# Optimization experiments

Hardware: AMD Instinct MI355X
Metric: run time of the kernel (lower is better)

The kernel has to match this reference:

```python
import jax, jax.numpy as jnp
import numpy as np

INPUT_DIM, HIDDEN_DIM, OUTPUT_DIM = 13, 256, 80


def setup_inputs() -> dict:
    key = jax.random.key(0)
    ks = jax.random.split(key, 5)
    x = jax.random.normal(ks[0], (64, 2048, INPUT_DIM), dtype=jnp.float32)
    # Xavier-uniform init like init_weights(); biases zero.
    def xavier(k, fan_in, fan_out):
        lim = np.sqrt(6.0 / (fan_in + fan_out)).astype(np.float32)
        return jax.random.uniform(k, (fan_in, fan_out), jnp.float32, -lim, lim)
    W1 = xavier(ks[1], INPUT_DIM, HIDDEN_DIM)
    W2 = xavier(ks[2], HIDDEN_DIM, HIDDEN_DIM)
    W3 = xavier(ks[3], HIDDEN_DIM, HIDDEN_DIM)
    W4 = xavier(ks[4], HIDDEN_DIM, OUTPUT_DIM)
    b1 = jnp.zeros((HIDDEN_DIM,), jnp.float32)
    b2 = jnp.zeros((HIDDEN_DIM,), jnp.float32)
    b3 = jnp.zeros((HIDDEN_DIM,), jnp.float32)
    b4 = jnp.zeros((OUTPUT_DIM,), jnp.float32)
    return {"x": x, "W1": W1, "b1": b1, "W2": W2, "b2": b2,
            "W3": W3, "b3": b3, "W4": W4, "b4": b4}


def reference(x, W1, b1, W2, b2, W3, b3, W4, b4):
    # Original loops over timesteps, but each timestep is an identical
    # Linear+ReLU stack -> collapse batch*seq into one batched matmul chain.
    h = jax.nn.relu(jnp.einsum('bsi,ih->bsh', x, W1) + b1)   # encoder L1
    h = jax.nn.relu(jnp.einsum('bsh,hk->bsk', h, W2) + b2)   # encoder L2
    h = jax.nn.relu(jnp.einsum('bsh,hk->bsk', h, W3) + b3)   # decoder L1
    out = jnp.einsum('bsh,ho->bso', h, W4) + b4              # decoder L2 (no ReLU)
    return out
```

## Files before the change

kernel.cpp:

```cpp
#include <hip/hip_runtime.h>


typedef _Float16 half_t;
typedef _Float16 half8 __attribute__((ext_vector_type(8)));
typedef float f32x16 __attribute__((ext_vector_type(16)));
typedef unsigned int uint4v __attribute__((ext_vector_type(4)));
typedef int int2v __attribute__((ext_vector_type(2)));

#define M_TOTAL (64*2048)

__global__ void prep_w(const float* __restrict__ W1, const float* __restrict__ W2,
                       const float* __restrict__ W3, const float* __restrict__ W4,
                       half_t* __restrict__ wp) {
    int tid = blockIdx.x * 256 + threadIdx.x;
    if (tid >= 312 * 512) return;
    int blk = tid >> 9, r = tid & 511;
    int lane = r >> 3, j = r & 7;
    const float* W; int K, N, nt, ks;
    if (blk < 8)        { W = W1; K = 13;  N = 256; nt = blk;              ks = 0; }
    else if (blk < 136) { W = W2; K = 256; N = 256; nt = (blk-8) >> 4;     ks = (blk-8) & 15; }
    else if (blk < 264) { W = W3; K = 256; N = 256; nt = (blk-136) >> 4;   ks = (blk-136) & 15; }
    else                { W = W4; K = 256; N = 80;  nt = (blk-264) >> 4;   ks = (blk-264) & 15; }
    int k = ks * 16 + (lane >> 5) * 8 + j;
    int n = nt * 32 + (lane & 31);
    float v = (k < K && n < N) ? W[k * N + n] : 0.f;
    wp[tid] = (half_t)v;
}


__device__ __forceinline__ unsigned int pkrtz(float a, float b) {
    auto p = __builtin_amdgcn_cvt_pkrtz(a, b);
    return __builtin_bit_cast(unsigned int, p);
}

typedef const __attribute__((address_space(1))) unsigned int guint_t;
typedef __attribute__((address_space(3))) unsigned int luint_t;

__device__ __forceinline__ void stage_strip(const half_t* __restrict__ g,
                                            half_t* l, int bytes, int tid) {
    const char* gc = (const char*)g;
    char* lc = (char*)l;
    const int go = tid * 16;
    const int lo = (tid >> 6) << 10;
#pragma unroll
    for (int r = 0; r < bytes; r += 4096) {
        __builtin_amdgcn_global_load_lds((guint_t*)(gc + r + go),
                                         (luint_t*)(lc + r + lo), 16, 0, 0);
    }
}

__device__ __forceinline__ int strip_off(int s) {
    if (s == 0)  return 0;
    if (s <= 4)  return (8   + (s - 1) * 32) * 512;
    if (s <= 8)  return (136 + (s - 5) * 32) * 512;
    if (s == 9)  return 264 * 512;
    return 296 * 512;
}

template <bool RELU>
__device__ __forceinline__ void repack_s(const f32x16& acc, int s,
                                         const float* biasnt, bool hi,
                                         unsigned int* Bw)
{
    float v[8];
#pragma unroll
    for (int q = 0; q < 8; ++q) {
        int f = (q & 3) + 8 * (q >> 2) + (hi ? 4 : 0);
        float t = acc[8 * s + q] + biasnt[16 * s + f];
        v[q] = RELU ? fmaxf(t, 0.f) : t;
    }
    unsigned int P0 = pkrtz(v[0], v[1]);
    unsigned int P1 = pkrtz(v[2], v[3]);
    unsigned int P2 = pkrtz(v[4], v[5]);
    unsigned int P3 = pkrtz(v[6], v[7]);
    int2v r02 = __builtin_amdgcn_permlane32_swap((int)P0, (int)P2, false, false);
    int2v r13 = __builtin_amdgcn_permlane32_swap((int)P1, (int)P3, false, false);
    Bw[0] = (unsigned int)r02.x;
    Bw[1] = (unsigned int)r13.x;
    Bw[2] = (unsigned int)r02.y;
    Bw[3] = (unsigned int)r13.y;
}

#define MFMA16(a, b, c) __builtin_amdgcn_mfma_f32_32x32x16_f16((a), (b), (c), 0, 0, 0)

__device__ __forceinline__ half8 bw_cast(const unsigned int* w) {
    uint4v t = { w[0], w[1], w[2], w[3] };
    return __builtin_bit_cast(half8, t);
}

template <bool RELU>
__device__ __forceinline__ void dense_phase(const half_t* sb,
                                            const unsigned int (&Bin)[2][16][4],
                                            unsigned int (&Bout)[2][16][4],
                                            int ntbase, const float* biasL,
                                            int lane, bool hi)
{
    f32x16 acc00 = {}, acc01 = {}, acc10 = {}, acc11 = {};
    __builtin_amdgcn_s_setprio(1);
#pragma unroll
    for (int ks = 0; ks < 16; ++ks) {
        half8 a0 = *(const half8*)(sb + ((ks * 64 + lane) << 3));
        half8 a1 = *(const half8*)(sb + 16 * 512 + ((ks * 64 + lane) << 3));
        half8 b0 = bw_cast(Bin[0][ks]);
        half8 b1 = bw_cast(Bin[1][ks]);
        acc00 = MFMA16(a0, b0, acc00);
        acc01 = MFMA16(a0, b1, acc01);
        acc10 = MFMA16(a1, b0, acc10);
        acc11 = MFMA16(a1, b1, acc11);
    }
    __builtin_amdgcn_s_setprio(0);
#pragma unroll
    for (int s = 0; s < 2; ++s) {
        repack_s<RELU>(acc00, s, biasL + ntbase * 32, hi, Bout[0][2 * ntbase + s]);
        repack_s<RELU>(acc01, s, biasL + ntbase * 32, hi, Bout[1][2 * ntbase + s]);
        repack_s<RELU>(acc10, s, biasL + (ntbase + 1) * 32, hi, Bout[0][2 * (ntbase + 1) + s]);
        repack_s<RELU>(acc11, s, biasL + (ntbase + 1) * 32, hi, Bout[1][2 * (ntbase + 1) + s]);
    }
}

__device__ __forceinline__ void out_phase2(const half_t* sb,
                                           const unsigned int (&Bin)[2][16][4],
                                           const float* bias4, float* __restrict__ out,
                                           int mb, int lane, bool hi)
{
    f32x16 acc00 = {}, acc01 = {}, acc10 = {}, acc11 = {};
    __builtin_amdgcn_s_setprio(1);
#pragma unroll
    for (int ks = 0; ks < 16; ++ks) {
        half8 a0 = *(const half8*)(sb + ((ks * 64 + lane) << 3));
        half8 a1 = *(const half8*)(sb + 16 * 512 + ((ks * 64 + lane) << 3));
        half8 b0 = bw_cast(Bin[0][ks]);
        half8 b1 = bw_cast(Bin[1][ks]);
        acc00 = MFMA16(a0, b0, acc00);
        acc01 = MFMA16(a0, b1, acc01);
        acc10 = MFMA16(a1, b0, acc10);
        acc11 = MFMA16(a1, b1, acc11);
    }
    __builtin_amdgcn_s_setprio(0);
#pragma unroll
    for (int ntL = 0; ntL < 2; ++ntL) {
#pragma unroll
        for (int g = 0; g < 2; ++g) {
            const f32x16& acc = ntL == 0 ? (g == 0 ? acc00 : acc01)
                                         : (g == 0 ? acc10 : acc11);
            float* orow = out + (long)(mb + g * 32 + (lane & 31)) * 80 + ntL * 32;
#pragma unroll
            for (int reg = 0; reg < 16; ++reg) {
                int rr = (reg & 3) + 8 * (reg >> 2) + (hi ? 4 : 0);
                orow[rr] = acc[reg] + bias4[ntL * 32 + rr];
            }
        }
    }
}

__device__ __forceinline__ void out_phase1(const half_t* sb,
                                           const unsigned int (&Bin)[2][16][4],
                                           const float* bias42, float* __restrict__ out,
                                           int mb, int lane, bool hi)
{
    f32x16 acc0 = {}, acc1 = {};
    __builtin_amdgcn_s_setprio(1);
#pragma unroll
    for (int ks = 0; ks < 16; ++ks) {
        half8 a = *(const half8*)(sb + ((ks * 64 + lane) << 3));
        acc0 = MFMA16(a, bw_cast(Bin[0][ks]), acc0);
        acc1 = MFMA16(a, bw_cast(Bin[1][ks]), acc1);
    }
    __builtin_amdgcn_s_setprio(0);
#pragma unroll
    for (int g = 0; g < 2; ++g) {
        const f32x16& acc = g == 0 ? acc0 : acc1;
        float* orow = out + (long)(mb + g * 32 + (lane & 31)) * 80 + 64;
#pragma unroll
        for (int reg = 0; reg < 8; ++reg) {
            int rr = (reg & 3) + 8 * (reg >> 2) + (hi ? 4 : 0);
            orow[rr] = acc[reg] + bias42[rr];
        }
    }
}

__global__ __attribute__((amdgpu_flat_work_group_size(256, 256), amdgpu_waves_per_eu(1)))
void mlp_mfma(
    const float* __restrict__ x, const half_t* __restrict__ wp,
    const float* __restrict__ b1, const float* __restrict__ b2,
    const float* __restrict__ b3, const float* __restrict__ b4,
    float* __restrict__ out)
{
    __shared__ half_t wbuf[2][16384];
    __shared__ float  bias_lds[864];

    const int tid  = threadIdx.x;
    const int lane = tid & 63;
    const int wave = tid >> 6;
    const bool hi  = lane >= 32;

    stage_strip(wp + strip_off(0), wbuf[0], 8192, tid);

    bias_lds[tid] = b1[tid];
    bias_lds[256 + tid] = b2[tid];
    bias_lds[512 + tid] = b3[tid];
    if (tid < 96) bias_lds[768 + tid] = (tid < 80) ? b4[tid] : 0.f;

    __syncthreads();

#pragma unroll
    for (int h = 0; h < 2; ++h) {
        const int mb = blockIdx.x * 512 + h * 256 + wave * 64;

        unsigned int Bx[2][4];
#pragma unroll
        for (int g = 0; g < 2; ++g) {
            const float* xp = x + (long)(mb + g * 32 + (lane & 31)) * 13;
            float xv[8];
            if (!hi) {
#pragma unroll
                for (int j = 0; j < 8; ++j) xv[j] = xp[j];
            } else {
#pragma unroll
                for (int j = 0; j < 5; ++j) xv[j] = xp[8 + j];
                xv[5] = xv[6] = xv[7] = 0.f;
            }
            Bx[g][0] = pkrtz(xv[0], xv[1]);
            Bx[g][1] = pkrtz(xv[2], xv[3]);
            Bx[g][2] = pkrtz(xv[4], xv[5]);
            Bx[g][3] = pkrtz(xv[6], xv[7]);
        }

        unsigned int BA[2][16][4], BB[2][16][4];

        {
            const int p = h * 11;
            stage_strip(wp + strip_off(1), wbuf[(p + 1) & 1], 32768, tid);
            __builtin_amdgcn_sched_barrier(0);
            const half_t* sb = &wbuf[p & 1][0];
            half8 bx0 = bw_cast(Bx[0]);
            half8 bx1 = bw_cast(Bx[1]);
#pragma unroll
            for (int nt = 0; nt < 8; ++nt) {
                half8 a = *(const half8*)(sb + nt * 512 + (lane << 3));
                f32x16 acc0 = {}, acc1 = {};
                acc0 = MFMA16(a, bx0, acc0);
                acc1 = MFMA16(a, bx1, acc1);
#pragma unroll
                for (int s = 0; s < 2; ++s) {
                    repack_s<true>(acc0, s, bias_lds + nt * 32, hi, BB[0][2 * nt + s]);
                    repack_s<true>(acc1, s, bias_lds + nt * 32, hi, BB[1][2 * nt + s]);
                }
            }
            __syncthreads();
        }

#pragma unroll
        for (int i = 0; i < 4; ++i) {
            const int p = h * 11 + 1 + i;
            stage_strip(wp + strip_off(2 + i), wbuf[(p + 1) & 1], 32768, tid);
            __builtin_amdgcn_sched_barrier(0);
            dense_phase<true>(&wbuf[p & 1][0], BB, BA, 2 * i, bias_lds + 256, lane, hi);
            __syncthreads();
        }

#pragma unroll
        for (int i = 0; i < 4; ++i) {
            const int p = h * 11 + 5 + i;
            stage_strip(wp + strip_off(6 + i), wbuf[(p + 1) & 1],
                        (6 + i == 9) ? 32768 : 32768, tid);
            __builtin_amdgcn_sched_barrier(0);
            dense_phase<true>(&wbuf[p & 1][0], BA, BB, 2 * i, bias_lds + 512, lane, hi);
            __syncthreads();
        }

        {
            const int p = h * 11 + 9;
            stage_strip(wp + strip_off(10), wbuf[(p + 1) & 1], 16384, tid);
            __builtin_amdgcn_sched_barrier(0);
            out_phase2(&wbuf[p & 1][0], BB, bias_lds + 768, out, mb, lane, hi);
            __syncthreads();
        }

        {
            const int p = h * 11 + 10;
            if (h == 0) {
                stage_strip(wp + strip_off(0), wbuf[(p + 1) & 1], 8192, tid);
                __builtin_amdgcn_sched_barrier(0);
            }
            out_phase1(&wbuf[p & 1][0], BB, bias_lds + 768 + 64, out, mb, lane, hi);
            __syncthreads();
        }
    }
}


extern "C" void kernel_launch(void* const* d_in, const int* in_sizes, int n_in,
                              void* d_out, int out_size, void* d_ws, size_t ws_size,
                              hipStream_t stream) {
    const float* x  = (const float*)d_in[0];
    const float* W1 = (const float*)d_in[1];
    const float* b1 = (const float*)d_in[2];
    const float* W2 = (const float*)d_in[3];
    const float* b2 = (const float*)d_in[4];
    const float* W3 = (const float*)d_in[5];
    const float* b3 = (const float*)d_in[6];
    const float* W4 = (const float*)d_in[7];
    const float* b4 = (const float*)d_in[8];
    float* out = (float*)d_out;

    half_t* wp = (half_t*)d_ws;

    hipLaunchKernelGGL(prep_w, dim3(624), dim3(256), 0, stream, W1, W2, W3, W4, wp);
    hipLaunchKernelGGL(mlp_mfma, dim3(M_TOTAL / 512), dim3(256), 0, stream,
                       x, wp, b1, b2, b3, b4, out);
}
```

Baseline: 60.58 us.

## Halve rows per block and allow two waves per EU for occupancy

Removes the two-half loop so each block handles 256 rows instead of 512. The grid doubles and the waves-per-EU hint rises from 1 to 2, so two blocks can share a CU and hide weight-staging and barrier latency. In exchange, each block stages the full weight strips from global memory, doubling L2 weight traffic. The register budget per wave is also halved, which risks spilling the large ping-pong activation arrays held in registers.

```diff
diff --git a/kernel.cpp b/kernel.cpp
--- a/kernel.cpp
+++ b/kernel.cpp
@@ -179,7 +179,7 @@
     }
 }
 
-__global__ __attribute__((amdgpu_flat_work_group_size(256, 256), amdgpu_waves_per_eu(1)))
+__global__ __attribute__((amdgpu_flat_work_group_size(256, 256), amdgpu_waves_per_eu(2)))
 void mlp_mfma(
     const float* __restrict__ x, const half_t* __restrict__ wp,
     const float* __restrict__ b1, const float* __restrict__ b2,
@@ -193,6 +193,7 @@
     const int lane = tid & 63;
     const int wave = tid >> 6;
     const bool hi  = lane >= 32;
+    const int mb   = blockIdx.x * 256 + wave * 64;
 
     stage_strip(wp + strip_off(0), wbuf[0], 8192, tid);
 
@@ -201,92 +202,77 @@
     bias_lds[512 + tid] = b3[tid];
     if (tid < 96) bias_lds[768 + tid] = (tid < 80) ? b4[tid] : 0.f;
 
+    unsigned int Bx[2][4];
+#pragma unroll
+    for (int g = 0; g < 2; ++g) {
+        const float* xp = x + (long)(mb + g * 32 + (lane & 31)) * 13;
+        float xv[8];
+        if (!hi) {
+#pragma unroll
+            for (int j = 0; j < 8; ++j) xv[j] = xp[j];
+        } else {
+#pragma unroll
+            for (int j = 0; j < 5; ++j) xv[j] = xp[8 + j];
+            xv[5] = xv[6] = xv[7] = 0.f;
+        }
+        Bx[g][0] = pkrtz(xv[0], xv[1]);
+        Bx[g][1] = pkrtz(xv[2], xv[3]);
+        Bx[g][2] = pkrtz(xv[4], xv[5]);
+        Bx[g][3] = pkrtz(xv[6], xv[7]);
+    }
+
     __syncthreads();
 
-#pragma unroll
-    for (int h = 0; h < 2; ++h) {
-        const int mb = blockIdx.x * 512 + h * 256 + wave * 64;
-
-        unsigned int Bx[2][4];
-#pragma unroll
-        for (int g = 0; g < 2; ++g) {
-            const float* xp = x + (long)(mb + g * 32 + (lane & 31)) * 13;
-            float xv[8];
-            if (!hi) {
-#pragma unroll
-                for (int j = 0; j < 8; ++j) xv[j] = xp[j];
-            } else {
-#pragma unroll
-                for (int j = 0; j < 5; ++j) xv[j] = xp[8 + j];
-                xv[5] = xv[6] = xv[7] = 0.f;
+    unsigned int BA[2][16][4], BB[2][16][4];
+
+    {
+        stage_strip(wp + strip_off(1), wbuf[1], 32768, tid);
+        __builtin_amdgcn_sched_barrier(0);
+        const half_t* sb = &wbuf[0][0];
+        half8 bx0 = bw_cast(Bx[0]);
+        half8 bx1 = bw_cast(Bx[1]);
+#pragma unroll
+        for (int nt = 0; nt < 8; ++nt) {
+            half8 a = *(const half8*)(sb + nt * 512 + (lane << 3));
+            f32x16 acc0 = {}, acc1 = {};
+            acc0 = MFMA16(a, bx0, acc0);
+            acc1 = MFMA16(a, bx1, acc1);
+#pragma unroll
+            for (int s = 0; s < 2; ++s) {
+                repack_s<true>(acc0, s, bias_lds + nt * 32, hi, BB[0][2 * nt + s]);
+                repack_s<true>(acc1, s, bias_lds + nt * 32, hi, BB[1][2 * nt + s]);
             }
-            Bx[g][0] = pkrtz(xv[0], xv[1]);
-            Bx[g][1] = pkrtz(xv[2], xv[3]);
-            Bx[g][2] = pkrtz(xv[4], xv[5]);
-            Bx[g][3] = pkrtz(xv[6], xv[7]);
-        }
-
-        unsigned int BA[2][16][4], BB[2][16][4];
-
-        {
-            const int p = h * 11;
-            stage_strip(wp + strip_off(1), wbuf[(p + 1) & 1], 32768, tid);
-            __builtin_amdgcn_sched_barrier(0);
-            const half_t* sb = &wbuf[p & 1][0];
-            half8 bx0 = bw_cast(Bx[0]);
-            half8 bx1 = bw_cast(Bx[1]);
-#pragma unroll
-            for (int nt = 0; nt < 8; ++nt) {
-                half8 a = *(const half8*)(sb + nt * 512 + (lane << 3));
-                f32x16 acc0 = {}, acc1 = {};
-                acc0 = MFMA16(a, bx0, acc0);
-                acc1 = MFMA16(a, bx1, acc1);
-#pragma unroll
-                for (int s = 0; s < 2; ++s) {
-                    repack_s<true>(acc0, s, bias_lds + nt * 32, hi, BB[0][2 * nt + s]);
-                    repack_s<true>(acc1, s, bias_lds + nt * 32, hi, BB[1][2 * nt + s]);
-                }
-            }
-            __syncthreads();
-        }
-
-#pragma unroll
-        for (int i = 0; i < 4; ++i) {
-            const int p = h * 11 + 1 + i;
-            stage_strip(wp + strip_off(2 + i), wbuf[(p + 1) & 1], 32768, tid);
-            __builtin_amdgcn_sched_barrier(0);
-            dense_phase<true>(&wbuf[p & 1][0], BB, BA, 2 * i, bias_lds + 256, lane, hi);
-            __syncthreads();
-        }
-
-#pragma unroll
-        for (int i = 0; i < 4; ++i) {
-            const int p = h * 11 + 5 + i;
-            stage_strip(wp + strip_off(6 + i), wbuf[(p + 1) & 1],
-                        (6 + i == 9) ? 32768 : 32768, tid);
-            __builtin_amdgcn_sched_barrier(0);
-            dense_phase<true>(&wbuf[p & 1][0], BA, BB, 2 * i, bias_lds + 512, lane, hi);
-            __syncthreads();
-        }
-
-        {
-            const int p = h * 11 + 9;
-            stage_strip(wp + strip_off(10), wbuf[(p + 1) & 1], 16384, tid);
-            __builtin_amdgcn_sched_barrier(0);
-            out_phase2(&wbuf[p & 1][0], BB, bias_lds + 768, out, mb, lane, hi);
-            __syncthreads();
-        }
-
-        {
-            const int p = h * 11 + 10;
-            if (h == 0) {
-                stage_strip(wp + strip_off(0), wbuf[(p + 1) & 1], 8192, tid);
-                __builtin_amdgcn_sched_barrier(0);
-            }
-            out_phase1(&wbuf[p & 1][0], BB, bias_lds + 768 + 64, out, mb, lane, hi);
-            __syncthreads();
-        }
-    }
+        }
+        __syncthreads();
+    }
+
+#pragma unroll
+    for (int i = 0; i < 4; ++i) {
+        const int p = 1 + i;
+        stage_strip(wp + strip_off(p + 1), wbuf[(p + 1) & 1], 32768, tid);
+        __builtin_amdgcn_sched_barrier(0);
+        dense_phase<true>(&wbuf[p & 1][0], BB, BA, 2 * i, bias_lds + 256, lane, hi);
+        __syncthreads();
+    }
+
+#pragma unroll
+    for (int i = 0; i < 4; ++i) {
+        const int p = 5 + i;
+        stage_strip(wp + strip_off(p + 1), wbuf[(p + 1) & 1],
+                    (p + 1 == 10) ? 16384 : 32768, tid);
+        __builtin_amdgcn_sched_barrier(0);
+        dense_phase<true>(&wbuf[p & 1][0], BA, BB, 2 * i, bias_lds + 512, lane, hi);
+        __syncthreads();
+    }
+
+    {
+        stage_strip(wp + strip_off(10), wbuf[0], 16384, tid);
+        __builtin_amdgcn_sched_barrier(0);
+        out_phase2(&wbuf[1][0], BB, bias_lds + 768, out, mb, lane, hi);
+        __syncthreads();
+    }
+
+    out_phase1(&wbuf[0][0], BB, bias_lds + 768 + 64, out, mb, lane, hi);
 }
 
 
@@ -307,6 +293,6 @@
     half_t* wp = (half_t*)d_ws;
 
     hipLaunchKernelGGL(prep_w, dim3(624), dim3(256), 0, stream, W1, W2, W3, W4, wp);
-    hipLaunchKernelGGL(mlp_mfma, dim3(M_TOTAL / 512), dim3(256), 0, stream,
+    hipLaunchKernelGGL(mlp_mfma, dim3(M_TOTAL / 256), dim3(256), 0, stream,
                        x, wp, b1, b2, b3, b4, out);
 }
```

After: 57.44 us. 1.05x faster.
